# Performance work log

Measured on AMD Instinct MI355X. Metric: run time of the kernel, lower is better.

Reference implementation:

```python
import jax, jax.numpy as jnp
import numpy as np

ALPHA = 0.2  # LeakyReLU negative slope
NEG_BIG = -9e15

def setup_inputs() -> dict:
    key = jax.random.key(0)
    k1, k2, k3, k4 = jax.random.split(key, 4)
    N, F_IN, F_OUT = 8192, 128, 128
    h = jax.random.normal(k1, (N, F_IN), dtype=jnp.float32)
    adj = jax.random.randint(k2, (N, N), 0, 2, dtype=jnp.int32)
    # xavier-uniform-ish params
    W = jax.random.normal(k3, (F_IN, F_OUT), dtype=jnp.float32) * (1.0 / np.sqrt(F_IN))
    a = jax.random.normal(k4, (2 * F_OUT, 1), dtype=jnp.float32) * (1.0 / np.sqrt(2 * F_OUT))
    return {"h": h, "adj": adj, "W": W, "a": a}

def reference(h, adj, W, a):
    # Wh: [N, F_OUT]
    Wh = h @ W
    F_out = Wh.shape[1]
    # a_input @ a == (Wh @ a1)_i + (Wh @ a2)_j  (same math, no N^2*2F tensor)
    a1 = a[:F_out, 0]   # [F_OUT]
    a2 = a[F_out:, 0]   # [F_OUT]
    e = (Wh @ a1)[:, None] + (Wh @ a2)[None, :]        # [N, N]
    e = jnp.where(e >= 0, e, ALPHA * e)                # LeakyReLU(0.2)
    scores = jnp.where(adj > 0, e, NEG_BIG)
    attention = jax.nn.softmax(scores, axis=1)         # row-wise
    # dropout skipped (eval mode / training=False)
    return attention @ Wh                              # [N, F_OUT]
```

## Files before the change

### kernel.cpp

```cpp
#include <hip/hip_runtime.h>
#include <hip/hip_bf16.h>

#define N 8192
#define FD 128
#define LOG2E 1.4426950408889634f

typedef __attribute__((ext_vector_type(4))) float f4;
typedef __attribute__((ext_vector_type(4))) int i32x4;
typedef __attribute__((ext_vector_type(4))) unsigned int u32x4;
typedef __attribute__((ext_vector_type(8))) __bf16 bf16x8;

__device__ __forceinline__ unsigned short bfbits(float x){
  __bf16 b = (__bf16)x;
  return __builtin_bit_cast(unsigned short, b);
}

__global__ __launch_bounds__(256) void k12_wh(const float* __restrict__ h,
                                              const float* __restrict__ W,
                                              const float* __restrict__ a,
                                              unsigned short* __restrict__ Bsw,
                                              float* __restrict__ s1L,
                                              float* __restrict__ s2L){
  __shared__ float Wl[64*128];
  __shared__ float hT[128*33];
  int t = threadIdx.x;
  int i0 = blockIdx.x * 32;
  {
    int r  = t >> 3;
    int k0 = (t & 7) * 16;
    const f4* src = (const f4*)&h[(size_t)(i0 + r)*FD + k0];
    #pragma unroll
    for (int q = 0; q < 4; ++q){
      f4 v = src[q];
      #pragma unroll
      for (int e = 0; e < 4; ++e) hT[(k0 + q*4 + e)*33 + r] = v[e];
    }
  }
  int f0 = (t & 31) * 4;
  int r0 = (t >> 5) * 4;
  float acc[4][4] = {};
  for (int half = 0; half < 2; ++half){
    __syncthreads();
    #pragma unroll
    for (int v = 0; v < 8; ++v){
      int idx = (v*256 + t)*4;
      *(f4*)&Wl[idx] = *(const f4*)&W[half*8192 + idx];
    }
    __syncthreads();
    for (int k2 = 0; k2 < 64; ++k2){
      f4 wv = *(const f4*)&Wl[k2*FD + f0];
      f4 hv = *(const f4*)&hT[(half*64 + k2)*33 + r0];
      #pragma unroll
      for (int ri = 0; ri < 4; ++ri)
        #pragma unroll
        for (int fi = 0; fi < 4; ++fi)
          acc[ri][fi] = __builtin_fmaf(hv[ri], wv[fi], acc[ri][fi]);
    }
  }
  int jblk = blockIdx.x;
  int n  = f0 >> 4;
  int fl = f0 & 15;
  #pragma unroll
  for (int ri = 0; ri < 4; ++ri){
    int k = r0 + ri;
    size_t base = (((size_t)jblk*8 + n)*64 + ((k>>3)<<4))*8 + (k&7);
    #pragma unroll
    for (int fi = 0; fi < 4; ++fi)
      Bsw[base + (size_t)(fl + fi)*8] = bfbits(acc[ri][fi]);
  }
  f4 a1v = *(const f4*)&a[f0];
  f4 a2v = *(const f4*)&a[FD + f0];
  float p1[4], p2[4];
  #pragma unroll
  for (int ri = 0; ri < 4; ++ri){
    p1[ri] = 0.f; p2[ri] = 0.f;
    #pragma unroll
    for (int fi = 0; fi < 4; ++fi){
      p1[ri] = __builtin_fmaf(acc[ri][fi], a1v[fi], p1[ri]);
      p2[ri] = __builtin_fmaf(acc[ri][fi], a2v[fi], p2[ri]);
    }
  }
  #pragma unroll
  for (int d = 1; d < 32; d <<= 1){
    #pragma unroll
    for (int ri = 0; ri < 4; ++ri){
      p1[ri] += __shfl_xor(p1[ri], d, 32);
      p2[ri] += __shfl_xor(p2[ri], d, 32);
    }
  }
  if ((t & 31) == 0){
    #pragma unroll
    for (int ri = 0; ri < 4; ++ri){
      s1L[i0 + r0 + ri] = p1[ri] * LOG2E;
      s2L[i0 + r0 + ri] = p2[ri] * LOG2E;
    }
  }
}

__global__ __launch_bounds__(256) void k3_max(const float* __restrict__ s2L,
                                              float* __restrict__ M2L){
  __shared__ float red[4];
  int t = threadIdx.x;
  float m = -3.0e38f;
  for (int i = t; i < N; i += 256) m = fmaxf(m, s2L[i]);
  #pragma unroll
  for (int d = 1; d < 64; d <<= 1) m = fmaxf(m, __shfl_xor(m, d, 64));
  if ((t & 63) == 0) red[t >> 6] = m;
  __syncthreads();
  if (t == 0) *M2L = fmaxf(fmaxf(red[0], red[1]), fmaxf(red[2], red[3]));
}

__global__ __launch_bounds__(256,2) void k4_flash(const int* __restrict__ adj,
    const unsigned short* __restrict__ Bsw,
    const float* __restrict__ s1L, const float* __restrict__ s2L,
    const float* __restrict__ M2p,
    float* __restrict__ partial, float* __restrict__ denomp, int njc){
  __shared__ unsigned char bswl[32768];
  __shared__ unsigned long long mkl[128][2];
  __shared__ float s2l[128];
  int t = threadIdx.x;
  int wv = t >> 6, lane = t & 63;
  int lrow = lane & 15, lgrp = lane >> 4;
  int bx = blockIdx.x;
  int jlen = N / njc;
  int jstart = blockIdx.y * jlen;
  int nmac = jlen >> 7;
  float M2 = *M2p;
  int i0w = bx*128 + wv*32;
  float s1a = s1L[i0w + lrow], s1b = s1L[i0w + 16 + lrow];
  float ea = s1a + M2, eb = s1b + M2;
  float maL = fmaxf(ea, 0.2f*ea);
  float mbL = fmaxf(eb, 0.2f*eb);

  f4 acc[2][8]; f4 accd[2];
  #pragma unroll
  for (int x = 0; x < 2; ++x){
    accd[x] = (f4){0.f,0.f,0.f,0.f};
    #pragma unroll
    for (int n = 0; n < 8; ++n) acc[x][n] = (f4){0.f,0.f,0.f,0.f};
  }
  u32x4 onesbits = (u32x4){0x3F803F80u,0x3F803F80u,0x3F803F80u,0x3F803F80u};
  bf16x8 ones = __builtin_bit_cast(bf16x8, onesbits);

  int srow = t >> 1;
  int shalf = t & 1;
  const i32x4* adjrow = (const i32x4*)(adj + (size_t)(bx*128 + srow)*N);

  for (int m = 0; m < nmac; ++m){
    int jb0 = jstart + m*128;
    i32x4 st[16];
    int ib = (jb0 + shalf*64) >> 2;
    #pragma unroll
    for (int e = 0; e < 16; ++e) st[e] = adjrow[ib + e];
    {
      const u32x4* src = (const u32x4*)(Bsw + (size_t)(jb0 >> 5) * 4096);
      u32x4* dst = (u32x4*)bswl;
      #pragma unroll
      for (int q = 0; q < 8; ++q)
        dst[q*256 + t] = src[q*256 + t];
    }
    if (t < 128) s2l[t] = s2L[jb0 + t];
    unsigned long long mv = 0ull;
    #pragma unroll
    for (int e = 0; e < 16; ++e){
      #pragma unroll
      for (int c = 0; c < 4; ++c)
        mv |= (st[e][c] != 0) ? (1ull << (e*4 + c)) : 0ull;
    }
    mkl[srow][shalf] = mv;
    __syncthreads();
    const unsigned char* mkb = (const unsigned char*)mkl;
    #pragma unroll
    for (int js = 0; js < 4; ++js){
      int jo = js*32 + lgrp*8;
      f4 ya = *(const f4*)&s2l[jo];
      f4 yb = *(const f4*)&s2l[jo+4];
      unsigned mba = mkb[(wv*32 + lrow)*16 + js*4 + lgrp];
      unsigned mbb = mkb[(wv*32 + 16 + lrow)*16 + js*4 + lgrp];
      u32x4 braw[8];
      #pragma unroll
      for (int n = 0; n < 8; ++n)
        braw[n] = *(const u32x4*)&bswl[((js*8 + n)*64 + lane)*16];
      bf16x8 fa, fb;
      #pragma unroll
      for (int e = 0; e < 8; ++e){
        float sj = (e < 4) ? ya[e] : yb[e-4];
        float xa = s1a + sj,               xb = s1b + sj;
        float la = fmaxf(xa, 0.2f*xa),     lb = fmaxf(xb, 0.2f*xb);
        float pa = ((mba>>e)&1u) ? __builtin_amdgcn_exp2f(la - maL) : 0.f;
        float pb = ((mbb>>e)&1u) ? __builtin_amdgcn_exp2f(lb - mbL) : 0.f;
        fa[e] = (__bf16)pa; fb[e] = (__bf16)pb;
      }
      accd[0] = __builtin_amdgcn_mfma_f32_16x16x32_bf16(fa, ones, accd[0], 0, 0, 0);
      accd[1] = __builtin_amdgcn_mfma_f32_16x16x32_bf16(fb, ones, accd[1], 0, 0, 0);
      #pragma unroll
      for (int n = 0; n < 8; ++n){
        bf16x8 bb = __builtin_bit_cast(bf16x8, braw[n]);
        acc[0][n] = __builtin_amdgcn_mfma_f32_16x16x32_bf16(fa, bb, acc[0][n], 0, 0, 0);
        acc[1][n] = __builtin_amdgcn_mfma_f32_16x16x32_bf16(fb, bb, acc[1][n], 0, 0, 0);
      }
    }
    __syncthreads();
  }

  if (lrow == 0){
    #pragma unroll
    for (int x = 0; x < 2; ++x)
      #pragma unroll
      for (int r = 0; r < 4; ++r)
        denomp[(size_t)blockIdx.y*N + i0w + x*16 + lgrp*4 + r] = accd[x][r];
  }
  float* pb = partial + (size_t)blockIdx.y * N * FD;
  #pragma unroll
  for (int x = 0; x < 2; ++x)
    #pragma unroll
    for (int n = 0; n < 8; ++n)
      #pragma unroll
      for (int r = 0; r < 4; ++r)
        pb[(size_t)(i0w + x*16 + lgrp*4 + r)*FD + n*16 + lrow] = acc[x][n][r];
}

__global__ __launch_bounds__(256) void k5_fin(const float* __restrict__ partial,
    const float* __restrict__ denomp, float* __restrict__ out, int njc){
  int g = blockIdx.x*256 + threadIdx.x;
  int i = g >> 7;
  float num = 0.f, den = 0.f;
  for (int c = 0; c < njc; ++c) num += partial[(size_t)c*N*FD + g];
  for (int c = 0; c < njc; ++c) den += denomp[(size_t)c*N + i];
  out[g] = num / den;
}

extern "C" void kernel_launch(void* const* d_in, const int* in_sizes, int n_in,
                              void* d_out, int out_size, void* d_ws, size_t ws_size,
                              hipStream_t stream){
  const float* h   = (const float*)d_in[0];
  const int*   adj = (const int*)d_in[1];
  const float* W   = (const float*)d_in[2];
  const float* a   = (const float*)d_in[3];
  float* out = (float*)d_out;
  char* ws = (char*)d_ws;

  unsigned short* Bsw = (unsigned short*)ws;
  float* s1L = (float*)(ws + (size_t)(6u<<20));
  float* s2L = (float*)(ws + (size_t)(6u<<20) + 32768);
  float* M2L = (float*)(ws + (size_t)(6u<<20) + 65536);
  float* denomp  = (float*)(ws + (size_t)(7u<<20));
  float* partial = (float*)(ws + (size_t)(8u<<20));

  size_t chunk = (size_t)N * FD * sizeof(float);
  int njc = 1;
  if (ws_size > ((size_t)(8u<<20))){
    size_t m = (ws_size - (size_t)(8u<<20)) / chunk;
    njc = (m >= 8) ? 8 : (m >= 4) ? 4 : (m >= 2) ? 2 : 1;
  }

  hipLaunchKernelGGL(k12_wh, dim3(256), dim3(256), 0, stream, h, W, a, Bsw, s1L, s2L);
  hipLaunchKernelGGL(k3_max, dim3(1),   dim3(256), 0, stream, s2L, M2L);
  hipLaunchKernelGGL(k4_flash, dim3(64, njc), dim3(256), 0, stream,
                     adj, Bsw, s1L, s2L, M2L, partial, denomp, njc);
  hipLaunchKernelGGL(k5_fin, dim3(N*FD/256), dim3(256), 0, stream, partial, denomp, out, njc);
}
```

Before: 448.2 us.

## Stream B tiles via global_load_lds, coalesce adj loads, raise occupancy and split count

The main attention kernel now copies the bf16 Wh tiles straight into LDS with global_load_lds, so they no longer pass through registers. The adjacency mask is read as coalesced row segments per wave and packed into a nibble layout in shared memory, replacing per-thread 64-bit masks. B-fragment register loads are split into two halves, and launch bounds ask for 4 blocks per CU to cut register pressure and raise occupancy. The column split can also go to 16 chunks when the workspace allows, which adds partial-sum traffic in the finalize kernel.

```diff
diff --git a/kernel.cpp b/kernel.cpp
--- a/kernel.cpp
+++ b/kernel.cpp
@@ -110,14 +110,14 @@
   if (t == 0) *M2L = fmaxf(fmaxf(red[0], red[1]), fmaxf(red[2], red[3]));
 }
 
-__global__ __launch_bounds__(256,2) void k4_flash(const int* __restrict__ adj,
+__global__ __launch_bounds__(256,4) void k4_flash(const int* __restrict__ adj,
     const unsigned short* __restrict__ Bsw,
     const float* __restrict__ s1L, const float* __restrict__ s2L,
     const float* __restrict__ M2p,
     float* __restrict__ partial, float* __restrict__ denomp, int njc){
-  __shared__ unsigned char bswl[32768];
-  __shared__ unsigned long long mkl[128][2];
-  __shared__ float s2l[128];
+  __shared__ __align__(16) unsigned char bswl[32768];
+  __shared__ __align__(16) unsigned char mknib[128*32];
+  __shared__ __align__(16) float s2l[128];
   int t = threadIdx.x;
   int wv = t >> 6, lane = t & 63;
   int lrow = lane & 15, lgrp = lane >> 4;
@@ -142,62 +142,84 @@
   u32x4 onesbits = (u32x4){0x3F803F80u,0x3F803F80u,0x3F803F80u,0x3F803F80u};
   bf16x8 ones = __builtin_bit_cast(bf16x8, onesbits);
 
-  int srow = t >> 1;
-  int shalf = t & 1;
-  const i32x4* adjrow = (const i32x4*)(adj + (size_t)(bx*128 + srow)*N);
+  const i32x4* adj4 = (const i32x4*)adj;
+  int sr2 = lane >> 5;
+  int sj  = lane & 31;
+  size_t abase = ((size_t)(bx*128 + wv*32 + sr2) * N) >> 2;
 
   for (int m = 0; m < nmac; ++m){
     int jb0 = jstart + m*128;
-    i32x4 st[16];
-    int ib = (jb0 + shalf*64) >> 2;
-    #pragma unroll
-    for (int e = 0; e < 16; ++e) st[e] = adjrow[ib + e];
-    {
-      const u32x4* src = (const u32x4*)(Bsw + (size_t)(jb0 >> 5) * 4096);
-      u32x4* dst = (u32x4*)bswl;
-      #pragma unroll
-      for (int q = 0; q < 8; ++q)
-        dst[q*256 + t] = src[q*256 + t];
-    }
-    if (t < 128) s2l[t] = s2L[jb0 + t];
-    unsigned long long mv = 0ull;
-    #pragma unroll
-    for (int e = 0; e < 16; ++e){
-      #pragma unroll
-      for (int c = 0; c < 4; ++c)
-        mv |= (st[e][c] != 0) ? (1ull << (e*4 + c)) : 0ull;
-    }
-    mkl[srow][shalf] = mv;
-    __syncthreads();
-    const unsigned char* mkb = (const unsigned char*)mkl;
+    const unsigned int* bg = (const unsigned int*)(Bsw + (size_t)(jb0 >> 5) * 4096);
+    #pragma unroll
+    for (int q = 0; q < 8; ++q){
+      int chunk = q*4 + wv;
+      __builtin_amdgcn_global_load_lds(
+        (const __attribute__((address_space(1))) unsigned int*)(bg + (size_t)(chunk*64 + lane)*4),
+        (__attribute__((address_space(3))) unsigned int*)(bswl + chunk*1024),
+        16, 0, 0);
+    }
+    size_t ab = abase + (size_t)(jb0 >> 2) + sj;
+    #pragma unroll
+    for (int eb = 0; eb < 4; ++eb){
+      i32x4 st[4];
+      #pragma unroll
+      for (int e = 0; e < 4; ++e)
+        st[e] = adj4[ab + (size_t)(eb*4 + e) * 4096];
+      #pragma unroll
+      for (int e = 0; e < 4; ++e){
+        unsigned nib = (st[e][0] != 0 ? 1u : 0u) | (st[e][1] != 0 ? 2u : 0u)
+                     | (st[e][2] != 0 ? 4u : 0u) | (st[e][3] != 0 ? 8u : 0u);
+        int rloc = wv*32 + (eb*4 + e)*2 + sr2;
+        mknib[rloc*32 + sj] = (unsigned char)nib;
+      }
+    }
+    if (t < 32) *(f4*)&s2l[t*4] = *(const f4*)&s2L[jb0 + t*4];
+    __syncthreads();
     #pragma unroll
     for (int js = 0; js < 4; ++js){
       int jo = js*32 + lgrp*8;
       f4 ya = *(const f4*)&s2l[jo];
       f4 yb = *(const f4*)&s2l[jo+4];
-      unsigned mba = mkb[(wv*32 + lrow)*16 + js*4 + lgrp];
-      unsigned mbb = mkb[(wv*32 + 16 + lrow)*16 + js*4 + lgrp];
-      u32x4 braw[8];
-      #pragma unroll
-      for (int n = 0; n < 8; ++n)
-        braw[n] = *(const u32x4*)&bswl[((js*8 + n)*64 + lane)*16];
+      int gb = (js*4 + lgrp)*2;
+      unsigned short ua = *(const unsigned short*)&mknib[(wv*32 + lrow)*32 + gb];
+      unsigned short ub = *(const unsigned short*)&mknib[(wv*32 + 16 + lrow)*32 + gb];
+      unsigned mba = (ua & 0xFu) | ((ua >> 4) & 0xF0u);
+      unsigned mbb = (ub & 0xFu) | ((ub >> 4) & 0xF0u);
       bf16x8 fa, fb;
       #pragma unroll
       for (int e = 0; e < 8; ++e){
-        float sj = (e < 4) ? ya[e] : yb[e-4];
-        float xa = s1a + sj,               xb = s1b + sj;
-        float la = fmaxf(xa, 0.2f*xa),     lb = fmaxf(xb, 0.2f*xb);
+        float sjv = (e < 4) ? ya[e] : yb[e-4];
+        float xa = s1a + sjv,            xb = s1b + sjv;
+        float la = fmaxf(xa, 0.2f*xa),   lb = fmaxf(xb, 0.2f*xb);
         float pa = ((mba>>e)&1u) ? __builtin_amdgcn_exp2f(la - maL) : 0.f;
         float pb = ((mbb>>e)&1u) ? __builtin_amdgcn_exp2f(lb - mbL) : 0.f;
         fa[e] = (__bf16)pa; fb[e] = (__bf16)pb;
       }
       accd[0] = __builtin_amdgcn_mfma_f32_16x16x32_bf16(fa, ones, accd[0], 0, 0, 0);
       accd[1] = __builtin_amdgcn_mfma_f32_16x16x32_bf16(fb, ones, accd[1], 0, 0, 0);
-      #pragma unroll
-      for (int n = 0; n < 8; ++n){
-        bf16x8 bb = __builtin_bit_cast(bf16x8, braw[n]);
-        acc[0][n] = __builtin_amdgcn_mfma_f32_16x16x32_bf16(fa, bb, acc[0][n], 0, 0, 0);
-        acc[1][n] = __builtin_amdgcn_mfma_f32_16x16x32_bf16(fb, bb, acc[1][n], 0, 0, 0);
+      {
+        u32x4 b0[4];
+        #pragma unroll
+        for (int n = 0; n < 4; ++n)
+          b0[n] = *(const u32x4*)&bswl[((js*8 + n)*64 + lane)*16];
+        #pragma unroll
+        for (int n = 0; n < 4; ++n){
+          bf16x8 bb = __builtin_bit_cast(bf16x8, b0[n]);
+          acc[0][n] = __builtin_amdgcn_mfma_f32_16x16x32_bf16(fa, bb, acc[0][n], 0, 0, 0);
+          acc[1][n] = __builtin_amdgcn_mfma_f32_16x16x32_bf16(fb, bb, acc[1][n], 0, 0, 0);
+        }
+      }
+      {
+        u32x4 b1[4];
+        #pragma unroll
+        for (int n = 0; n < 4; ++n)
+          b1[n] = *(const u32x4*)&bswl[((js*8 + 4 + n)*64 + lane)*16];
+        #pragma unroll
+        for (int n = 0; n < 4; ++n){
+          bf16x8 bb = __builtin_bit_cast(bf16x8, b1[n]);
+          acc[0][4+n] = __builtin_amdgcn_mfma_f32_16x16x32_bf16(fa, bb, acc[0][4+n], 0, 0, 0);
+          acc[1][4+n] = __builtin_amdgcn_mfma_f32_16x16x32_bf16(fb, bb, acc[1][4+n], 0, 0, 0);
+        }
       }
     }
     __syncthreads();
@@ -251,7 +273,7 @@
   int njc = 1;
   if (ws_size > ((size_t)(8u<<20))){
     size_t m = (ws_size - (size_t)(8u<<20)) / chunk;
-    njc = (m >= 8) ? 8 : (m >= 4) ? 4 : (m >= 2) ? 2 : 1;
+    njc = (m >= 16) ? 16 : (m >= 8) ? 8 : (m >= 4) ? 4 : (m >= 2) ? 2 : 1;
   }
 
   hipLaunchKernelGGL(k12_wh, dim3(256), dim3(256), 0, stream, h, W, a, Bsw, s1L, s2L);
```

Result: faster. 437.0 us (-2.5%).
